# Performance work log

Hardware: AMD Instinct MI355X
Metric: run time of the kernel (lower is better)

The kernel has to match this reference:

```python
import jax, jax.numpy as jnp
import numpy as np

B, S, H, HEADS, STEP = 128, 256, 128, 8, 1


def setup_inputs() -> dict:
    key = jax.random.key(0)
    ks = jax.random.split(key, 20)
    rn = lambda k, shape: jax.random.normal(k, shape, dtype=jnp.float32) * 0.1
    return {
        "A": jax.random.uniform(ks[0], (B, S, 2 * S), dtype=jnp.float32),
        "hidden": jax.random.normal(ks[1], (B, S, H), dtype=jnp.float32),
        "mask": jnp.ones((B, S), dtype=jnp.int32),
        "w_ih": rn(ks[2], (3 * H, 2 * H)),
        "w_hh": rn(ks[3], (3 * H, H)),
        "b_ih": rn(ks[4], (3 * H,)),
        "b_hh": rn(ks[5], (3 * H,)),
        "b_iah": rn(ks[6], (H,)),
        "b_oah": rn(ks[7], (H,)),
        "W_ein": rn(ks[8], (H, H)), "b_ein": rn(ks[9], (H,)),
        "W_eout": rn(ks[10], (H, H)), "b_eout": rn(ks[11], (H,)),
        "W_q0": rn(ks[12], (H, H)), "b_q0": rn(ks[13], (H,)),
        "W_q1": rn(ks[14], (H, H)), "b_q1": rn(ks[15], (H,)),
        "W_q2": rn(ks[16], (H, H)), "b_q2": rn(ks[17], (H,)),
    }


def _forward(A, hidden, mask, w_ih, w_hh, b_ih, b_hh, b_iah, b_oah,
             W_ein, b_ein, W_eout, b_eout, W_q0, b_q0, W_q1, b_q1, W_q2, b_q2):
    b, s, h = hidden.shape
    dk = h // HEADS
    # ---- GNN: gated graph propagation (GRU cell over adjacency messages) ----
    for _ in range(STEP):
        msg_in = A[:, :, :s] @ (hidden @ W_ein.T + b_ein) + b_iah    # [B,S,H]
        msg_out = A[:, :, s:] @ (hidden @ W_eout.T + b_eout) + b_oah  # [B,S,H]
        inputs = jnp.concatenate([msg_in, msg_out], axis=2)           # [B,S,2H]
        gi = inputs @ w_ih.T + b_ih                                   # [B,S,3H]
        gh = hidden @ w_hh.T + b_hh                                   # [B,S,3H]
        i_r, i_i, i_n = jnp.split(gi, 3, axis=2)
        h_r, h_i, h_n = jnp.split(gh, 3, axis=2)
        resetgate = jax.nn.sigmoid(i_r + h_r)
        inputgate = jax.nn.sigmoid(i_i + h_i)
        newgate = jnp.tanh(i_n + resetgate * h_n)
        hidden = hidden - inputgate * (hidden - newgate)
    # ---- query: hidden state of the last valid item in each session ----
    last_idx = jnp.sum(mask, axis=1) - 1
    ht1 = hidden[jnp.arange(b), last_idx]                             # [B,H]
    # ---- LastAttenion: sigmoid score + double softmax readout ----
    q0 = (ht1 @ W_q0.T + b_q0).reshape(b, HEADS, dk)                  # [B,h,dk]
    q1 = (hidden @ W_q1.T + b_q1).reshape(b, s, HEADS, dk).transpose(0, 2, 1, 3)
    q2 = (hidden @ W_q2.T + b_q2).reshape(b, s, HEADS, dk).transpose(0, 2, 1, 3)
    # q0 is expanded over the query axis, so every score row is identical
    alpha = jax.nn.sigmoid(jnp.einsum('bhd,bhjd->bhj', q0, q1))        # [B,h,S]
    alpha = jnp.broadcast_to(alpha[:, :, None, :], (b, HEADS, s, s))   # [B,h,S,S]
    alpha = jax.nn.softmax(alpha, axis=-1)
    row_keep = (mask > 0)[:, None, :, None]                            # [B,1,S,1]
    alpha = jnp.where(row_keep, alpha, -jnp.inf)
    alpha = jax.nn.softmax(2.0 * alpha, axis=1)                        # over heads
    alpha = jnp.where(row_keep, alpha, 0.0)  # guard fully-masked rows (torch would NaN)
    x = jnp.einsum('bhij,bhjd->bhid', alpha, q2)                       # [B,h,S,dk]
    x = x.transpose(0, 2, 1, 3).reshape(b, s, h)                       # [B,S,H]
    a = jnp.sum(x * mask[:, :, None].astype(x.dtype), axis=1)          # [B,H]
    return a


def reference(A, hidden, mask, w_ih, w_hh, b_ih, b_hh, b_iah, b_oah,
              W_ein, b_ein, W_eout, b_eout, W_q0, b_q0, W_q1, b_q1, W_q2, b_q2):
    return _forward(A, hidden, mask, w_ih, w_hh, b_ih, b_hh, b_iah, b_oah,
                    W_ein, b_ein, W_eout, b_eout, W_q0, b_q0, W_q1, b_q1, W_q2, b_q2)
```

## Files before the change

kernel.cpp:

```cpp
#include <hip/hip_runtime.h>
#include <cstdint>
#include <cstddef>

#define BB   128
#define SS   256
#define HH   128
#define NH   8
#define DKK  16

typedef unsigned short u16;
typedef __attribute__((ext_vector_type(8))) short   sh8;
typedef __attribute__((ext_vector_type(4))) float   f32x4;

__device__ __forceinline__ float sigmoidf_(float x) { return 1.f / (1.f + expf(-x)); }

__device__ __forceinline__ u16 f2bf(float x) {
    union { float f; unsigned int u; } v; v.f = x;
    unsigned int r = (v.u + 0x7fffu + ((v.u >> 16) & 1u)) >> 16;
    return (u16)r;
}
__device__ __forceinline__ float bf2f(u16 u) {
    union { unsigned int u; float f; } v; v.u = ((unsigned int)u) << 16;
    return v.f;
}

#define BKk 32
#define PK  40

template<int XMODE, int OMODE>
__global__ __launch_bounds__(256) void gemm_mfma(
    const void* __restrict__ Xa, const void* __restrict__ Xc, int ldx, int ldx1, int ksplit,
    long long sXb, long long sXh,
    const u16* __restrict__ Bw, int ldb, long long sBb, long long sBh,
    const float* __restrict__ bias,
    void* __restrict__ Out, long long ldo, long long sOb, long long sOh,
    int K, const float* __restrict__ hid)
{
    __shared__ __align__(16) char smem[2 * 128 * PK * 2];
    u16* As = (u16*)smem;
    u16* Bs = (u16*)(smem + 128 * PK * 2);

    const int t  = threadIdx.x;
    const int bm = blockIdx.x * 128;
    const int bn = blockIdx.y * 128;
    const long long zb = blockIdx.z >> 1, zh = blockIdx.z & 1;

    const u16* Bp = Bw + zb * sBb + zh * sBh;

    const int wave = t >> 6, lane = t & 63;
    const int wr = (wave >> 1) * 64, wc = (wave & 1) * 64;
    const int fm = lane & 15, fq = lane >> 4;

    f32x4 acc[4][4] = {};

    const int r0  = t >> 2, kk0 = (t & 3) * 8;
    const int r1  = t >> 3, kk1 = (t & 7) * 4;

    for (int k0 = 0; k0 < K; k0 += BKk) {
        if (XMODE == 1 || (XMODE == 3 && k0 >= ksplit)) {
            const float* Xf;
            int kb, ld;
            if (XMODE == 1) {
                Xf = (const float*)Xa + zb * sXb + zh * sXh; kb = k0; ld = ldx;
            } else {
                Xf = (const float*)Xc; kb = k0 - ksplit; ld = ldx1;
            }
            #pragma unroll
            for (int c = 0; c < 4; c++) {
                int r = r1 + 32 * c;
                float4 v = *(const float4*)(Xf + (long long)(bm + r) * ld + kb + kk1);
                ushort4 w = { f2bf(v.x), f2bf(v.y), f2bf(v.z), f2bf(v.w) };
                *(ushort4*)&As[r * PK + kk1] = w;
            }
        } else {
            #pragma unroll
            for (int c = 0; c < 2; c++) {
                int r = r0 + 64 * c;
                const u16* src = (const u16*)Xa + (long long)(bm + r) * ldx + k0 + kk0;
                uint4 v = *(const uint4*)src;
                *(uint4*)&As[r * PK + kk0] = v;
            }
        }
        #pragma unroll
        for (int c = 0; c < 2; c++) {
            int r = r0 + 64 * c;
            uint4 v = *(const uint4*)(Bp + (long long)(bn + r) * ldb + k0 + kk0);
            *(uint4*)&Bs[r * PK + kk0] = v;
        }
        __syncthreads();

        sh8 af[4], bfr[4];
        #pragma unroll
        for (int i = 0; i < 4; i++) af[i]  = *(const sh8*)&As[(wr + i * 16 + fm) * PK + fq * 8];
        #pragma unroll
        for (int j = 0; j < 4; j++) bfr[j] = *(const sh8*)&Bs[(wc + j * 16 + fm) * PK + fq * 8];
        #pragma unroll
        for (int i = 0; i < 4; i++)
            #pragma unroll
            for (int j = 0; j < 4; j++)
                acc[i][j] = __builtin_amdgcn_mfma_f32_16x16x32_bf16(af[i], bfr[j], acc[i][j], 0, 0, 0);
        __syncthreads();
    }

    if (OMODE != 3) {
        #pragma unroll
        for (int j = 0; j < 4; j++) {
            const int col = bn + wc + j * 16 + fm;
            const float bj = bias ? bias[col] : 0.f;
            #pragma unroll
            for (int i = 0; i < 4; i++) {
                const int row0 = bm + wr + i * 16 + fq * 4;
                if (OMODE == 1) {
                    u16* O = (u16*)Out + zb * sOb + zh * sOh;
                    #pragma unroll
                    for (int r = 0; r < 4; r++)
                        O[(long long)(row0 + r) * ldo + col] = f2bf(acc[i][j][r] + bj);
                } else {
                    u16* O = (u16*)Out + zb * sOb + zh * sOh;
                    ushort4 w = { f2bf(acc[i][j][0] + bj), f2bf(acc[i][j][1] + bj),
                                  f2bf(acc[i][j][2] + bj), f2bf(acc[i][j][3] + bj) };
                    *(ushort4*)&O[(long long)col * ldo + row0] = w;
                }
            }
        }
    } else {
        float* g4s = (float*)smem;
        const int chbase = bn >> 2;
        const int s_t = t >> 3;
        const int cq  = t & 7;
        u16* O = (u16*)Out;
        const int sbase = (wr ? 16 : 0) + fq * 4;
        #pragma unroll
        for (int i = 0; i < 4; i++) {
            #pragma unroll
            for (int j = 0; j < 4; j++) {
                const int q = wc + j * 16 + fm;
                const float bj = bias[bn + q];
                #pragma unroll
                for (int r = 0; r < 4; r++)
                    g4s[(sbase + r) * 132 + q] = acc[i][j][r] + bj;
            }
            __syncthreads();
            {
                const int grow = bm + i * 16 + (s_t < 16 ? s_t : s_t + 48);
                const float4 hv = *(const float4*)&hid[(long long)grow * HH + chbase + 4 * cq];
                const float hvv[4] = { hv.x, hv.y, hv.z, hv.w };
                ushort4 w;
                u16* wp = (u16*)&w;
                #pragma unroll
                for (int m = 0; m < 4; m++) {
                    f32x4 gv = *(const f32x4*)&g4s[s_t * 132 + 16 * cq + 4 * m];
                    float rg = sigmoidf_(gv[0]);
                    float ig = sigmoidf_(gv[1]);
                    float ng = tanhf(gv[2] + rg * gv[3]);
                    wp[m] = f2bf(hvv[m] - ig * (hvv[m] - ng));
                }
                *(ushort4*)&O[(long long)grow * ldo + chbase + 4 * cq] = w;
            }
            __syncthreads();
        }
    }
}

__global__ __launch_bounds__(256) void k_prepw(
    const float* __restrict__ w_ih, const float* __restrict__ w_hh,
    const float* __restrict__ b_ih, const float* __restrict__ b_hh,
    const float* __restrict__ b_iah, const float* __restrict__ b_oah,
    const float* __restrict__ W_ein, const float* __restrict__ b_ein,
    const float* __restrict__ W_eout, const float* __restrict__ b_eout,
    const float* __restrict__ W_q1, const float* __restrict__ b_q1,
    const float* __restrict__ W_q2, const float* __restrict__ b_q2,
    u16* __restrict__ W2bf, float* __restrict__ bias2,
    u16* __restrict__ Wcat, float* __restrict__ biascat,
    u16* __restrict__ Wq12, float* __restrict__ biasq12)
{
    int idx = blockIdx.x * 256 + threadIdx.x;
    if (idx < 512 * 384) {
        int np = idx / 384, kk = idx % 384;
        int c = np >> 2, g = np & 3;
        float v;
        if (g < 2)       v = (kk < 256) ? w_ih[(g * 128 + c) * 256 + kk]
                                        : w_hh[(g * 128 + c) * 128 + kk - 256];
        else if (g == 2) v = (kk < 256) ? w_ih[(256 + c) * 256 + kk] : 0.f;
        else             v = (kk < 256) ? 0.f : w_hh[(256 + c) * 128 + kk - 256];
        W2bf[idx] = f2bf(v);
    }
    if (idx < 256 * 128) {
        int n = idx >> 7, k = idx & 127;
        Wcat[idx] = f2bf(n < 128 ? W_ein[n * 128 + k] : W_eout[(n - 128) * 128 + k]);
        Wq12[idx] = f2bf(n < 128 ? W_q1[n * 128 + k]  : W_q2[(n - 128) * 128 + k]);
    }
    if (idx < 512) {
        int np = idx, c = np >> 2, g = np & 3;
        float s;
        if (g < 2)       s = b_ih[g * 128 + c] + b_hh[g * 128 + c];
        else if (g == 2) s = b_ih[256 + c];
        else             s = b_hh[256 + c];
        if (g < 3) {
            int n = (g < 2) ? g * 128 + c : 256 + c;
            for (int k = 0; k < 128; k++)
                s += w_ih[n * 256 + k] * b_iah[k] + w_ih[n * 256 + 128 + k] * b_oah[k];
        }
        bias2[np] = s;
    }
    if (idx < 256) {
        biascat[idx] = idx < 128 ? b_ein[idx] : b_eout[idx - 128];
        biasq12[idx] = idx < 128 ? b_q1[idx]  : b_q2[idx - 128];
    }
}

__global__ __launch_bounds__(256) void k_tail(
    const u16* __restrict__ hnew_bf, const int* __restrict__ mask,
    const u16* __restrict__ q12, const float* __restrict__ Wq0,
    const float* __restrict__ bq0, float* __restrict__ out)
{
    const int b = blockIdx.x, t = threadIdx.x;
    __shared__ float red[256];
    __shared__ float hs[HH];
    __shared__ float q0s[HH];
    __shared__ float p_s[NH][SS];
    __shared__ float w_s[NH][SS];
    __shared__ int s_nv;

    red[t] = (float)mask[b * SS + t];
    __syncthreads();
    for (int off = 128; off > 0; off >>= 1) {
        if (t < off) red[t] += red[t + off];
        __syncthreads();
    }
    if (t == 0) s_nv = (int)red[0];
    __syncthreads();
    const int nv = s_nv;
    const int last = (nv - 1) & (SS - 1);

    if (t < HH) hs[t] = bf2f(hnew_bf[((size_t)b * SS + last) * HH + t]);
    __syncthreads();

    {
        const int n = t & 127, kh = t >> 7;
        const float* w = Wq0 + (size_t)n * HH + kh * 64;
        float s = 0.f;
        #pragma unroll 16
        for (int k = 0; k < 64; k++) s += hs[kh * 64 + k] * w[k];
        red[t] = s;
    }
    __syncthreads();
    if (t < HH) q0s[t] = red[t] + red[t + 128] + bq0[t];
    __syncthreads();

    {
        const u16* q1r = q12 + ((size_t)b * SS + t) * 256;
        #pragma unroll
        for (int h = 0; h < NH; h++) {
            float s = 0.f;
            #pragma unroll
            for (int d = 0; d < DKK; d++) s += q0s[h * DKK + d] * bf2f(q1r[h * DKK + d]);
            p_s[h][t] = sigmoidf_(s);
        }
    }
    __syncthreads();

    {
        const int h = t >> 5, l = t & 31;
        float v[8], m = -1e30f;
        #pragma unroll
        for (int u = 0; u < 8; u++) { v[u] = p_s[h][l * 8 + u]; m = fmaxf(m, v[u]); }
        #pragma unroll
        for (int msk = 1; msk < 32; msk <<= 1) m = fmaxf(m, __shfl_xor(m, msk, 32));
        float sum = 0.f;
        #pragma unroll
        for (int u = 0; u < 8; u++) { v[u] = expf(v[u] - m); sum += v[u]; }
        #pragma unroll
        for (int msk = 1; msk < 32; msk <<= 1) sum += __shfl_xor(sum, msk, 32);
        const float inv = 1.f / sum;
        #pragma unroll
        for (int u = 0; u < 8; u++) p_s[h][l * 8 + u] = v[u] * inv;
    }
    __syncthreads();

    {
        float e[NH], den = 0.f;
        #pragma unroll
        for (int h = 0; h < NH; h++) { e[h] = expf(2.f * p_s[h][t]); den += e[h]; }
        const float inv = 1.f / den;
        #pragma unroll
        for (int h = 0; h < NH; h++) w_s[h][t] = e[h] * inv;
    }
    __syncthreads();

    {
        const int col = t & 127, jh = t >> 7;
        const int h = col >> 4;
        const u16* q2b = q12 + (size_t)b * SS * 256 + 128 + col;
        float acc = 0.f;
        for (int j = jh * 128; j < jh * 128 + 128; j++)
            acc += w_s[h][j] * bf2f(q2b[(size_t)j * 256]);
        red[t] = acc;
    }
    __syncthreads();
    if (t < HH) out[(size_t)b * HH + t] = (red[t] + red[t + 128]) * (float)nv;
}

extern "C" void kernel_launch(void* const* d_in, const int* in_sizes, int n_in,
                              void* d_out, int out_size, void* d_ws, size_t ws_size,
                              hipStream_t stream)
{
    const float* A      = (const float*)d_in[0];
    const float* hidden = (const float*)d_in[1];
    const int*   mask   = (const int*)d_in[2];
    const float* w_ih   = (const float*)d_in[3];
    const float* w_hh   = (const float*)d_in[4];
    const float* b_ih   = (const float*)d_in[5];
    const float* b_hh   = (const float*)d_in[6];
    const float* b_iah  = (const float*)d_in[7];
    const float* b_oah  = (const float*)d_in[8];
    const float* W_ein  = (const float*)d_in[9];
    const float* b_ein  = (const float*)d_in[10];
    const float* W_eout = (const float*)d_in[11];
    const float* b_eout = (const float*)d_in[12];
    const float* W_q0   = (const float*)d_in[13];
    const float* b_q0   = (const float*)d_in[14];
    const float* W_q1   = (const float*)d_in[15];
    const float* b_q1   = (const float*)d_in[16];
    const float* W_q2   = (const float*)d_in[17];
    const float* b_q2   = (const float*)d_in[18];
    float* out = (float*)d_out;
    char* ws = (char*)d_ws;

    u16*   Et      = (u16*)(ws + 0);
    u16*   Mbuf    = (u16*)(ws + 16777216);
    u16*   q12bf   = (u16*)(ws + 0);
    u16*   hnew_bf = (u16*)(ws + 33554432);
    u16*   W2bf    = (u16*)(ws + 41943040);
    u16*   Wcat    = (u16*)(ws + 42336256);
    u16*   Wq12    = (u16*)(ws + 42401792);
    float* bias2   = (float*)(ws + 42467328);
    float* biascat = (float*)(ws + 42469376);
    float* biasq12 = (float*)(ws + 42470400);

    k_prepw<<<768, 256, 0, stream>>>(w_ih, w_hh, b_ih, b_hh, b_iah, b_oah,
                                     W_ein, b_ein, W_eout, b_eout,
                                     W_q1, b_q1, W_q2, b_q2,
                                     W2bf, bias2, Wcat, biascat, Wq12, biasq12);

    gemm_mfma<1, 2><<<dim3(256, 2, 1), 256, 0, stream>>>(
        hidden, nullptr, HH, 0, 0, 0, 0,
        Wcat, HH, 0, 0, biascat,
        Et, 32768, 0, 0, HH, nullptr);

    gemm_mfma<1, 1><<<dim3(2, 1, 256), 256, 0, stream>>>(
        A, nullptr, 512, 0, 0, 131072LL, 256LL,
        Et, 32768, 256LL, 128LL * 32768LL, nullptr,
        Mbuf, 256, 65536LL, 128LL, SS, nullptr);

    gemm_mfma<3, 3><<<dim3(256, 4, 1), 256, 0, stream>>>(
        Mbuf, hidden, 256, HH, 256, 0, 0,
        W2bf, 384, 0, 0, bias2,
        hnew_bf, HH, 0, 0, 384, hidden);

    gemm_mfma<0, 1><<<dim3(256, 2, 1), 256, 0, stream>>>(
        hnew_bf, nullptr, HH, 0, 0, 0, 0,
        Wq12, HH, 0, 0, biasq12,
        q12bf, 256, 0, 0, HH, nullptr);

    k_tail<<<BB, 256, 0, stream>>>(hnew_bf, mask, q12bf, W_q0, b_q0, out);
}
```

Measured before the change: 254.6 us.

## Prefetch next K-tile into registers and pre-convert hidden to bf16 once

The GEMM main loop now issues global loads for the next K-tile into registers right after the barrier, so they overlap with the MFMA work on the current tile. The hidden tensor is converted to bf16 once inside the weight-prep kernel, and the first and third GEMMs read it as bf16 instead of converting fp32 per tile. The GEMM also gets a launch_bounds occupancy hint. The prefetch raises register pressure, and the prep kernel now launches many more blocks to cover the hidden conversion.

```diff
diff --git a/kernel.cpp b/kernel.cpp
--- a/kernel.cpp
+++ b/kernel.cpp
@@ -28,7 +28,7 @@
 #define PK  40
 
 template<int XMODE, int OMODE>
-__global__ __launch_bounds__(256) void gemm_mfma(
+__global__ __launch_bounds__(256, 4) void gemm_mfma(
     const void* __restrict__ Xa, const void* __restrict__ Xc, int ldx, int ldx1, int ksplit,
     long long sXb, long long sXh,
     const u16* __restrict__ Bw, int ldb, long long sBb, long long sBh,
@@ -56,38 +56,55 @@
     const int r0  = t >> 2, kk0 = (t & 3) * 8;
     const int r1  = t >> 3, kk1 = (t & 7) * 4;
 
+    uint4  pX[2];
+    float4 pF[4];
+    uint4  pB[2];
+
+    auto load_x = [&](int k0) {
+        if (XMODE == 1) {
+            const float* Xf = (const float*)Xa + zb * sXb + zh * sXh;
+            #pragma unroll
+            for (int c = 0; c < 4; c++)
+                pF[c] = *(const float4*)(Xf + (long long)(bm + r1 + 32 * c) * ldx + k0 + kk1);
+        } else if (XMODE == 2 && k0 >= ksplit) {
+            #pragma unroll
+            for (int c = 0; c < 2; c++)
+                pX[c] = *(const uint4*)((const u16*)Xc +
+                        (long long)(bm + r0 + 64 * c) * ldx1 + (k0 - ksplit) + kk0);
+        } else {
+            #pragma unroll
+            for (int c = 0; c < 2; c++)
+                pX[c] = *(const uint4*)((const u16*)Xa +
+                        (long long)(bm + r0 + 64 * c) * ldx + k0 + kk0);
+        }
+    };
+    auto load_b = [&](int k0) {
+        #pragma unroll
+        for (int c = 0; c < 2; c++)
+            pB[c] = *(const uint4*)(Bp + (long long)(bn + r0 + 64 * c) * ldb + k0 + kk0);
+    };
+
+    load_x(0);
+    load_b(0);
+
     for (int k0 = 0; k0 < K; k0 += BKk) {
-        if (XMODE == 1 || (XMODE == 3 && k0 >= ksplit)) {
-            const float* Xf;
-            int kb, ld;
-            if (XMODE == 1) {
-                Xf = (const float*)Xa + zb * sXb + zh * sXh; kb = k0; ld = ldx;
-            } else {
-                Xf = (const float*)Xc; kb = k0 - ksplit; ld = ldx1;
-            }
+        if (XMODE == 1) {
             #pragma unroll
             for (int c = 0; c < 4; c++) {
-                int r = r1 + 32 * c;
-                float4 v = *(const float4*)(Xf + (long long)(bm + r) * ld + kb + kk1);
-                ushort4 w = { f2bf(v.x), f2bf(v.y), f2bf(v.z), f2bf(v.w) };
-                *(ushort4*)&As[r * PK + kk1] = w;
+                ushort4 w = { f2bf(pF[c].x), f2bf(pF[c].y), f2bf(pF[c].z), f2bf(pF[c].w) };
+                *(ushort4*)&As[(r1 + 32 * c) * PK + kk1] = w;
             }
         } else {
             #pragma unroll
-            for (int c = 0; c < 2; c++) {
-                int r = r0 + 64 * c;
-                const u16* src = (const u16*)Xa + (long long)(bm + r) * ldx + k0 + kk0;
-                uint4 v = *(const uint4*)src;
-                *(uint4*)&As[r * PK + kk0] = v;
-            }
-        }
-        #pragma unroll
-        for (int c = 0; c < 2; c++) {
-            int r = r0 + 64 * c;
-            uint4 v = *(const uint4*)(Bp + (long long)(bn + r) * ldb + k0 + kk0);
-            *(uint4*)&Bs[r * PK + kk0] = v;
-        }
+            for (int c = 0; c < 2; c++)
+                *(uint4*)&As[(r0 + 64 * c) * PK + kk0] = pX[c];
+        }
+        #pragma unroll
+        for (int c = 0; c < 2; c++)
+            *(uint4*)&Bs[(r0 + 64 * c) * PK + kk0] = pB[c];
         __syncthreads();
+
+        if (k0 + BKk < K) { load_x(k0 + BKk); load_b(k0 + BKk); }
 
         sh8 af[4], bfr[4];
         #pragma unroll
@@ -163,6 +180,7 @@
 }
 
 __global__ __launch_bounds__(256) void k_prepw(
+    const float* __restrict__ hidden, u16* __restrict__ h_bf,
     const float* __restrict__ w_ih, const float* __restrict__ w_hh,
     const float* __restrict__ b_ih, const float* __restrict__ b_hh,
     const float* __restrict__ b_iah, const float* __restrict__ b_oah,
@@ -175,6 +193,11 @@
     u16* __restrict__ Wq12, float* __restrict__ biasq12)
 {
     int idx = blockIdx.x * 256 + threadIdx.x;
+    {
+        float4 v = ((const float4*)hidden)[idx];
+        ushort4 w = { f2bf(v.x), f2bf(v.y), f2bf(v.z), f2bf(v.w) };
+        ((ushort4*)h_bf)[idx] = w;
+    }
     if (idx < 512 * 384) {
         int np = idx / 384, kk = idx % 384;
         int c = np >> 2, g = np & 3;
@@ -331,20 +354,22 @@
     u16*   Mbuf    = (u16*)(ws + 16777216);
     u16*   q12bf   = (u16*)(ws + 0);
     u16*   hnew_bf = (u16*)(ws + 33554432);
-    u16*   W2bf    = (u16*)(ws + 41943040);
-    u16*   Wcat    = (u16*)(ws + 42336256);
-    u16*   Wq12    = (u16*)(ws + 42401792);
-    float* bias2   = (float*)(ws + 42467328);
-    float* biascat = (float*)(ws + 42469376);
-    float* biasq12 = (float*)(ws + 42470400);
-
-    k_prepw<<<768, 256, 0, stream>>>(w_ih, w_hh, b_ih, b_hh, b_iah, b_oah,
-                                     W_ein, b_ein, W_eout, b_eout,
-                                     W_q1, b_q1, W_q2, b_q2,
-                                     W2bf, bias2, Wcat, biascat, Wq12, biasq12);
-
-    gemm_mfma<1, 2><<<dim3(256, 2, 1), 256, 0, stream>>>(
-        hidden, nullptr, HH, 0, 0, 0, 0,
+    u16*   h_bf    = (u16*)(ws + 41943040);
+    u16*   W2bf    = (u16*)(ws + 50331648);
+    u16*   Wcat    = (u16*)(ws + 50724864);
+    u16*   Wq12    = (u16*)(ws + 50790400);
+    float* bias2   = (float*)(ws + 50855936);
+    float* biascat = (float*)(ws + 50857984);
+    float* biasq12 = (float*)(ws + 50859008);
+
+    k_prepw<<<4096, 256, 0, stream>>>(hidden, h_bf,
+                                      w_ih, w_hh, b_ih, b_hh, b_iah, b_oah,
+                                      W_ein, b_ein, W_eout, b_eout,
+                                      W_q1, b_q1, W_q2, b_q2,
+                                      W2bf, bias2, Wcat, biascat, Wq12, biasq12);
+
+    gemm_mfma<0, 2><<<dim3(256, 2, 1), 256, 0, stream>>>(
+        h_bf, nullptr, HH, 0, 0, 0, 0,
         Wcat, HH, 0, 0, biascat,
         Et, 32768, 0, 0, HH, nullptr);
 
@@ -353,8 +378,8 @@
         Et, 32768, 256LL, 128LL * 32768LL, nullptr,
         Mbuf, 256, 65536LL, 128LL, SS, nullptr);
 
-    gemm_mfma<3, 3><<<dim3(256, 4, 1), 256, 0, stream>>>(
-        Mbuf, hidden, 256, HH, 256, 0, 0,
+    gemm_mfma<2, 3><<<dim3(256, 4, 1), 256, 0, stream>>>(
+        Mbuf, h_bf, 256, HH, 256, 0, 0,
         W2bf, 384, 0, 0, bias2,
         hnew_bf, HH, 0, 0, 384, hidden);
 
```

Result: slower. 314.6 us (+23.6%).
